# Performance work log

Measured on AMD Instinct MI355X. Metric: run time of the kernel, lower is better.

Reference implementation:

```python
import jax, jax.numpy as jnp
import numpy as np

N_EMBD = 2048
HEAD_DIM = 128
N_CTX = 2048
BATCH = 8
SEQ = 2048


def setup_inputs() -> dict:
    key = jax.random.key(0)
    ks = jax.random.split(key, 7)
    s = 1.0 / np.sqrt(N_EMBD)
    x = jax.random.normal(ks[0], (BATCH, SEQ, N_EMBD), dtype=jnp.float32)
    # torch Linear params: weight (out, in), bias (out,)
    Wq = jax.random.uniform(ks[1], (HEAD_DIM, N_EMBD), jnp.float32, -s, s)
    bq = jax.random.uniform(ks[2], (HEAD_DIM,), jnp.float32, -s, s)
    Wk = jax.random.uniform(ks[3], (HEAD_DIM, N_EMBD), jnp.float32, -s, s)
    bk = jax.random.uniform(ks[4], (HEAD_DIM,), jnp.float32, -s, s)
    Wv = jax.random.uniform(ks[5], (HEAD_DIM, N_EMBD), jnp.float32, -s, s)
    bv = jax.random.uniform(ks[6], (HEAD_DIM,), jnp.float32, -s, s)
    return {"x": x, "Wq": Wq, "bq": bq, "Wk": Wk, "bk": bk, "Wv": Wv, "bv": bv}


def reference(x, Wq, bq, Wk, bk, Wv, bv):
    # projections: y = x @ W^T + b
    q = jnp.einsum('bse,de->bsd', x, Wq) + bq  # (B, S, D)
    k = jnp.einsum('bse,de->bsd', x, Wk) + bk
    v = jnp.einsum('bse,de->bsd', x, Wv) + bv
    seq = x.shape[1]
    scores = jnp.einsum('bqd,bkd->bqk', q, k)  # (B, S, S)
    # causal mask: strictly-upper-triangular positions set to -inf (before scaling, as in source)
    causal = jnp.triu(jnp.ones((seq, seq), dtype=bool), k=1)
    scores = jnp.where(causal[None, :, :], -jnp.inf, scores)
    # NOTE: source scales by sqrt(seq_size), not sqrt(head_dim)
    weight = jax.nn.softmax(scores / jnp.sqrt(jnp.float32(seq)), axis=-1)
    return jnp.einsum('bqk,bkd->bqd', weight, v)
```

## Files before the change

### kernel.cpp

```cpp
#include <hip/hip_runtime.h>
#include <cmath>

#define BATCH 8
#define SEQ   2048
#define NEMB  2048
#define HD    128
#define NROWS (BATCH * SEQ)

typedef __bf16 v8bf __attribute__((ext_vector_type(8)));
typedef float  f32x4 __attribute__((ext_vector_type(4)));

union U8 { v8bf v; __bf16 b[8]; unsigned short e[8]; };
union F4 { f32x4 v; float f[4]; };

__device__ inline void async16(void* lds, const void* g) {
  __builtin_amdgcn_global_load_lds(
      (const __attribute__((address_space(1))) unsigned int*)g,
      (__attribute__((address_space(3))) unsigned int*)lds, 16, 0, 0);
}

__device__ inline v8bf cvt8(float4 a, float4 b) {
  U8 u;
  u.b[0] = (__bf16)a.x; u.b[1] = (__bf16)a.y; u.b[2] = (__bf16)a.z; u.b[3] = (__bf16)a.w;
  u.b[4] = (__bf16)b.x; u.b[5] = (__bf16)b.y; u.b[6] = (__bf16)b.z; u.b[7] = (__bf16)b.w;
  return u.v;
}

__global__ __launch_bounds__(256) void wconv_kernel(
    const float* __restrict__ Wq, const float* __restrict__ Wk,
    const float* __restrict__ Wv, __bf16* __restrict__ out) {
  const int id = blockIdx.x;
  const int proj = id >> 6, blk = id & 63;
  const float* __restrict__ W = proj == 0 ? Wq : proj == 1 ? Wk : Wv;
  __bf16* __restrict__ o = out + (size_t)proj * (HD * NEMB);
  const int base = blk * 4096 + threadIdx.x * 16;
  const float4* s = (const float4*)(W + base);
  float4 f0 = s[0], f1 = s[1], f2 = s[2], f3 = s[3];
  *(v8bf*)(o + base) = cvt8(f0, f1);
  *(v8bf*)(o + base + 8) = cvt8(f2, f3);
}

__global__ __launch_bounds__(256, 3) void qkv_proj_kernel(
    const float* __restrict__ x, const __bf16* __restrict__ Wb,
    const float* __restrict__ bq, const float* __restrict__ bk,
    const float* __restrict__ bv,
    __bf16* __restrict__ Qb, __bf16* __restrict__ Kb, __bf16* __restrict__ Vb)
{
  const int bid0 = blockIdx.x;
  const int bid = ((bid0 & 7) * 96) + (bid0 >> 3);
  const int mt = bid / 3;
  const int proj = bid % 3;
  const __bf16* __restrict__ W = Wb + (size_t)proj * (HD * NEMB);
  const float* __restrict__ bias = proj == 0 ? bq : proj == 1 ? bk : bv;
  __bf16* __restrict__ Out = proj == 0 ? Qb : proj == 1 ? Kb : Vb;
  const int m0 = mt * 64;

  __shared__ float  Asm[64 * 64];
  __shared__ __bf16 Bsm[128 * 64];

  const int t = threadIdx.x, lane = t & 63, w = t >> 6;
  const int wm = w >> 1, wn = w & 1;
  const int hi = lane >> 4, lo = lane & 15;

  const float* pa[4];
  const __bf16* pb[4];
  char* la[4];
  char* lb[4];
#pragma unroll
  for (int i = 0; i < 4; ++i) {
    {
      const int r = (w * 4 + i) * 4 + (lane >> 4);
      const int c = (lane & 15) ^ (r & 7);
      pa[i] = x + (size_t)(m0 + r) * NEMB + c * 4;
      la[i] = (char*)Asm + (w * 4 + i) * 1024;
    }
    {
      const int r = (w * 4 + i) * 8 + (lane >> 3);
      const int c = (lane & 7) ^ (r & 7);
      pb[i] = W + (size_t)r * NEMB + c * 8;
      lb[i] = (char*)Bsm + (w * 4 + i) * 1024;
    }
  }

  f32x4 acc[2][4];
  const f32x4 fz = {0.f, 0.f, 0.f, 0.f};
#pragma unroll
  for (int m = 0; m < 2; ++m)
#pragma unroll
    for (int n = 0; n < 4; ++n) acc[m][n] = fz;

  for (int tt = 0; tt < NEMB / 64; ++tt) {
    const int k0 = tt * 64;
    __syncthreads();
#pragma unroll
    for (int i = 0; i < 4; ++i) async16(la[i], pa[i] + k0);
#pragma unroll
    for (int i = 0; i < 4; ++i) async16(lb[i], pb[i] + k0);
    __syncthreads();

#pragma unroll
    for (int kk = 0; kk < 2; ++kk) {
      v8bf a[2], b[4];
#pragma unroll
      for (int m = 0; m < 2; ++m) {
        const int r = wm * 32 + m * 16 + lo;
        const int s = kk * 8 + hi * 2;
        const char* rowp = (const char*)Asm + r * 256;
        F4 a0, a1;
        a0.v = *(const f32x4*)(rowp + (((s)     ^ (r & 7)) << 4));
        a1.v = *(const f32x4*)(rowp + (((s + 1) ^ (r & 7)) << 4));
        U8 u;
#pragma unroll
        for (int q = 0; q < 4; ++q) {
          u.b[q]     = (__bf16)a0.f[q];
          u.b[q + 4] = (__bf16)a1.f[q];
        }
        a[m] = u.v;
      }
#pragma unroll
      for (int n = 0; n < 4; ++n) {
        const int r = wn * 64 + n * 16 + lo;
        const int kc = kk * 4 + hi;
        b[n] = *(const v8bf*)((const char*)Bsm + r * 128 + ((kc ^ (r & 7)) << 4));
      }
#pragma unroll
      for (int m = 0; m < 2; ++m)
#pragma unroll
        for (int n = 0; n < 4; ++n)
          acc[m][n] = __builtin_amdgcn_mfma_f32_16x16x32_bf16(a[m], b[n], acc[m][n], 0, 0, 0);
    }
  }

#pragma unroll
  for (int n = 0; n < 4; ++n) {
    const int col = wn * 64 + n * 16 + lo;
    const float bi = bias[col];
#pragma unroll
    for (int m = 0; m < 2; ++m) {
#pragma unroll
      for (int r = 0; r < 4; ++r) {
        const int row = m0 + wm * 32 + m * 16 + hi * 4 + r;
        Out[(size_t)row * HD + col] = (__bf16)(acc[m][n][r] + bi);
      }
    }
  }
}

__global__ __launch_bounds__(256) void attn_kernel(
    const __bf16* __restrict__ Qb, const __bf16* __restrict__ Kb,
    const __bf16* __restrict__ Vb, float* __restrict__ Opart,
    float* __restrict__ Ml)
{
  const int bid0 = blockIdx.x;
  const int bid = ((bid0 & 7) << 6) + (bid0 >> 3);
  const int b = bid >> 6;
  const int qs = bid & 63;
  const int qt = qs >> 1;
  const int s  = qs & 1;
  const int q0 = qt * 64;
  const int half = (qt + 2) >> 1;
  const int kv_beg = s ? half : 0;
  const int kv_end = s ? (qt + 1) : half;
  const int nst = kv_end - kv_beg;

  const int t = threadIdx.x, lane = t & 63, w = t >> 6;
  const int hi = lane >> 4, lo = lane & 15;

  __shared__ __bf16 Ksm[2][64 * 128];
  __shared__ __bf16 Vtsm[2][128 * 64];
  __shared__ __bf16 Psm[4][16 * 64];

  v8bf aQ[4];
  {
    const __bf16* qp = Qb + ((size_t)(b * SEQ + q0 + w * 16 + lo)) * HD + hi * 8;
#pragma unroll
    for (int kk = 0; kk < 4; ++kk) aQ[kk] = *(const v8bf*)(qp + kk * 32);
  }

  const __bf16* kga[4];
#pragma unroll
  for (int i = 0; i < 4; ++i) {
    const int r = (w * 4 + i) * 4 + (lane >> 4);
    const int c = (lane & 15) ^ (r & 7);
    kga[i] = Kb + ((size_t)(b * SEQ) + r) * HD + c * 8;
  }

  const int keyg = t >> 4, dg = t & 15;
  U8 vv[4];

  f32x4 accO[8];
  const f32x4 fz = {0.f, 0.f, 0.f, 0.f};
#pragma unroll
  for (int n = 0; n < 8; ++n) accO[n] = fz;
  float m_s[4], l_s[4];
#pragma unroll
  for (int r = 0; r < 4; ++r) { m_s[r] = -INFINITY; l_s[r] = 0.f; }

  const float scale = 0.022097086912079608f;

  if (nst > 0) {
    auto STAGE_K = [&](int kv, int buf) {
      const size_t off = (size_t)kv * 64 * HD;
      char* kb = (char*)&Ksm[buf][0];
#pragma unroll
      for (int i = 0; i < 4; ++i) async16(kb + (w * 4 + i) * 1024, kga[i] + off);
    };
    auto LOAD_V = [&](int kv) {
      const __bf16* vp = Vb + ((size_t)(b * SEQ + kv * 64 + keyg * 4)) * HD + dg * 8;
#pragma unroll
      for (int j = 0; j < 4; ++j) vv[j].v = *(const v8bf*)(vp + (size_t)j * HD);
    };
    auto WRITE_VT = [&](int buf) {
      char* vb2 = (char*)&Vtsm[buf][0];
#pragma unroll
      for (int dd = 0; dd < 8; ++dd) {
        const int d = (dd + dg) & 7;
        ushort4 pk = make_ushort4(vv[0].e[d], vv[1].e[d], vv[2].e[d], vv[3].e[d]);
        const int row = dg * 8 + d;
        *(ushort4*)(vb2 + row * 128 + ((keyg * 8) ^ ((row & 7) << 4))) = pk;
      }
    };

    STAGE_K(kv_beg, 0);
    LOAD_V(kv_beg);
    WRITE_VT(0);
    __syncthreads();

    for (int t2 = 0; t2 < nst; ++t2) {
      const int kv = kv_beg + t2;
      const int cur = t2 & 1;
      const bool more = (t2 + 1 < nst);
      if (more) { STAGE_K(kv + 1, cur ^ 1); LOAD_V(kv + 1); }

      f32x4 accS[4];
#pragma unroll
      for (int n = 0; n < 4; ++n) accS[n] = fz;
      const char* ksm = (const char*)&Ksm[cur][0];
#pragma unroll
      for (int kk = 0; kk < 4; ++kk) {
        const int cb = kk * 64 + hi * 16;
        v8bf bk[4];
#pragma unroll
        for (int n = 0; n < 4; ++n) {
          const int r = n * 16 + lo;
          bk[n] = *(const v8bf*)(ksm + r * 256 + (cb ^ ((r & 7) << 4)));
        }
#pragma unroll
        for (int n = 0; n < 4; ++n)
          accS[n] = __builtin_amdgcn_mfma_f32_16x16x32_bf16(aQ[kk], bk[n], accS[n], 0, 0, 0);
      }

      float sv[4][4];
      const bool diag = (kv == qt);
#pragma unroll
      for (int n = 0; n < 4; ++n)
#pragma unroll
        for (int r = 0; r < 4; ++r) {
          float v = accS[n][r] * scale;
          if (diag) {
            const int key = kv * 64 + n * 16 + lo;
            const int qr = q0 + w * 16 + hi * 4 + r;
            if (key > qr) v = -INFINITY;
          }
          sv[n][r] = v;
        }

      float mx[4];
#pragma unroll
      for (int r = 0; r < 4; ++r) {
        mx[r] = fmaxf(fmaxf(sv[0][r], sv[1][r]), fmaxf(sv[2][r], sv[3][r]));
#pragma unroll
        for (int off = 1; off < 16; off <<= 1)
          mx[r] = fmaxf(mx[r], __shfl_xor(mx[r], off));
      }
      float corr[4], p[4][4], rs[4];
#pragma unroll
      for (int r = 0; r < 4; ++r) {
        const float mnew = fmaxf(m_s[r], mx[r]);
        corr[r] = __expf(m_s[r] - mnew);
        m_s[r] = mnew;
        rs[r] = 0.f;
      }
#pragma unroll
      for (int n = 0; n < 4; ++n)
#pragma unroll
        for (int r = 0; r < 4; ++r) {
          p[n][r] = __expf(sv[n][r] - m_s[r]);
          rs[r] += p[n][r];
        }
#pragma unroll
      for (int r = 0; r < 4; ++r) {
#pragma unroll
        for (int off = 1; off < 16; off <<= 1) rs[r] += __shfl_xor(rs[r], off);
        l_s[r] = l_s[r] * corr[r] + rs[r];
      }
#pragma unroll
      for (int n = 0; n < 8; ++n)
#pragma unroll
        for (int r = 0; r < 4; ++r) accO[n][r] *= corr[r];

#pragma unroll
      for (int n = 0; n < 4; ++n)
#pragma unroll
        for (int r = 0; r < 4; ++r) {
          const int row = hi * 4 + r;
          __bf16 h = (__bf16)p[n][r];
          *(unsigned short*)((char*)&Psm[w][0] + row * 128 +
                             (((n * 16 + lo) * 2) ^ ((row & 7) << 4))) =
              __builtin_bit_cast(unsigned short, h);
        }

      if (more) WRITE_VT(cur ^ 1);

      const char* vsm = (const char*)&Vtsm[cur][0];
#pragma unroll
      for (int k2 = 0; k2 < 2; ++k2) {
        const int cb = k2 * 64 + hi * 16;
        const v8bf aP = *(const v8bf*)((const char*)&Psm[w][0] + lo * 128 + (cb ^ ((lo & 7) << 4)));
#pragma unroll
        for (int n = 0; n < 8; ++n) {
          const int r = n * 16 + lo;
          const v8bf bv = *(const v8bf*)(vsm + r * 128 + (cb ^ ((r & 7) << 4)));
          accO[n] = __builtin_amdgcn_mfma_f32_16x16x32_bf16(aP, bv, accO[n], 0, 0, 0);
        }
      }
      if (more) __syncthreads();
    }
  }

#pragma unroll
  for (int r = 0; r < 4; ++r) {
    const int qr = q0 + w * 16 + hi * 4 + r;
    float* op = Opart + ((size_t)s * NROWS + b * SEQ + qr) * HD + lo;
#pragma unroll
    for (int n = 0; n < 8; ++n) op[n * 16] = accO[n][r];
    if (lo == 0) {
      float* mlp = Ml + ((size_t)s * NROWS + b * SEQ + qr) * 2;
      mlp[0] = m_s[r];
      mlp[1] = l_s[r];
    }
  }
}

__global__ __launch_bounds__(256) void combine_kernel(
    const float* __restrict__ Opart, const float* __restrict__ Ml,
    float* __restrict__ out)
{
  const int idx = blockIdx.x * 256 + threadIdx.x;
  const int row = idx >> 1, h = idx & 1;
  const float m0 = Ml[(size_t)row * 2],           l0 = Ml[(size_t)row * 2 + 1];
  const float m1 = Ml[((size_t)NROWS + row) * 2], l1 = Ml[((size_t)NROWS + row) * 2 + 1];
  const float M = fmaxf(m0, m1);
  const float e0 = __expf(m0 - M), e1 = __expf(m1 - M);
  const float inv = 1.f / (l0 * e0 + l1 * e1);
  const float4* p0 = (const float4*)(Opart + (size_t)row * HD + h * 64);
  const float4* p1 = (const float4*)(Opart + ((size_t)NROWS + row) * HD + h * 64);
  float4* po = (float4*)(out + (size_t)row * HD + h * 64);
#pragma unroll
  for (int j = 0; j < 16; ++j) {
    float4 a = p0[j], c = p1[j];
    float4 r;
    r.x = (a.x * e0 + c.x * e1) * inv;
    r.y = (a.y * e0 + c.y * e1) * inv;
    r.z = (a.z * e0 + c.z * e1) * inv;
    r.w = (a.w * e0 + c.w * e1) * inv;
    po[j] = r;
  }
}

extern "C" void kernel_launch(void* const* d_in, const int* in_sizes, int n_in,
                              void* d_out, int out_size, void* d_ws, size_t ws_size,
                              hipStream_t stream) {
  const float* x  = (const float*)d_in[0];
  const float* Wq = (const float*)d_in[1];
  const float* bq = (const float*)d_in[2];
  const float* Wk = (const float*)d_in[3];
  const float* bk = (const float*)d_in[4];
  const float* Wv = (const float*)d_in[5];
  const float* bv = (const float*)d_in[6];
  float* out = (float*)d_out;

  __bf16* Qb = (__bf16*)d_ws;
  __bf16* Kb = Qb + (size_t)NROWS * HD;
  __bf16* Vb = Kb + (size_t)NROWS * HD;
  __bf16* Wb = Vb + (size_t)NROWS * HD;
  float*  Opart = (float*)(Wb + (size_t)3 * HD * NEMB);
  float*  Ml    = Opart + (size_t)2 * NROWS * HD;

  wconv_kernel<<<dim3(3 * 64), dim3(256), 0, stream>>>(Wq, Wk, Wv, Wb);
  qkv_proj_kernel<<<dim3(256 * 3), dim3(256), 0, stream>>>(
      x, Wb, bq, bk, bv, Qb, Kb, Vb);
  attn_kernel<<<dim3(BATCH * 32 * 2), dim3(256), 0, stream>>>(Qb, Kb, Vb, Opart, Ml);
  combine_kernel<<<dim3(NROWS * 2 / 256), dim3(256), 0, stream>>>(Opart, Ml, out);
}
```

Before: 124.9 us.

## Prepack weights into MFMA fragment layout and load B directly to registers

The weight conversion kernel now writes bf16 weights in the per-lane MFMA fragment order, so the projection kernel can read B operands straight from global memory into registers with coalesced 16-byte loads. This removes the B staging in shared memory. B fragments are double-buffered in registers across k-tiles so the next tile's loads overlap the current MFMAs. The cost is more registers under a 3-blocks-per-SM launch bound and more frequent barriers, since the loop now syncs four times per pair of tiles. Weight loads also bypass LDS reuse and rely on cache hits across blocks.

```diff
diff --git a/kernel.cpp b/kernel.cpp
--- a/kernel.cpp
+++ b/kernel.cpp
@@ -26,22 +26,27 @@
   return u.v;
 }
 
-__global__ __launch_bounds__(256) void wconv_kernel(
+__global__ __launch_bounds__(256) void wpack_kernel(
     const float* __restrict__ Wq, const float* __restrict__ Wk,
     const float* __restrict__ Wv, __bf16* __restrict__ out) {
-  const int id = blockIdx.x;
-  const int proj = id >> 6, blk = id & 63;
-  const float* __restrict__ W = proj == 0 ? Wq : proj == 1 ? Wk : Wv;
-  __bf16* __restrict__ o = out + (size_t)proj * (HD * NEMB);
-  const int base = blk * 4096 + threadIdx.x * 16;
-  const float4* s = (const float4*)(W + base);
-  float4 f0 = s[0], f1 = s[1], f2 = s[2], f3 = s[3];
-  *(v8bf*)(o + base) = cvt8(f0, f1);
-  *(v8bf*)(o + base + 8) = cvt8(f2, f3);
+  const int idx = blockIdx.x * 256 + threadIdx.x;
+  const int lane = idx & 63;
+  const int g = idx >> 6;
+  const int fg = g & 7;
+  const int tt = (g >> 3) & 31;
+  const int wn = (g >> 8) & 1;
+  const int p  = g >> 9;
+  const int n = fg >> 1, kk = fg & 1;
+  const int row = wn * 64 + n * 16 + (lane & 15);
+  const int k   = tt * 64 + kk * 32 + (lane >> 4) * 8;
+  const float* __restrict__ W = p == 0 ? Wq : p == 1 ? Wk : Wv;
+  const float4* s = (const float4*)(W + (size_t)row * NEMB + k);
+  float4 f0 = s[0], f1 = s[1];
+  *(v8bf*)(out + (size_t)idx * 8) = cvt8(f0, f1);
 }
 
 __global__ __launch_bounds__(256, 3) void qkv_proj_kernel(
-    const float* __restrict__ x, const __bf16* __restrict__ Wb,
+    const float* __restrict__ x, const __bf16* __restrict__ Wpack,
     const float* __restrict__ bq, const float* __restrict__ bk,
     const float* __restrict__ bv,
     __bf16* __restrict__ Qb, __bf16* __restrict__ Kb, __bf16* __restrict__ Vb)
@@ -50,37 +55,27 @@
   const int bid = ((bid0 & 7) * 96) + (bid0 >> 3);
   const int mt = bid / 3;
   const int proj = bid % 3;
-  const __bf16* __restrict__ W = Wb + (size_t)proj * (HD * NEMB);
   const float* __restrict__ bias = proj == 0 ? bq : proj == 1 ? bk : bv;
   __bf16* __restrict__ Out = proj == 0 ? Qb : proj == 1 ? Kb : Vb;
   const int m0 = mt * 64;
 
-  __shared__ float  Asm[64 * 64];
-  __shared__ __bf16 Bsm[128 * 64];
+  __shared__ float Asm[64 * 64];
 
   const int t = threadIdx.x, lane = t & 63, w = t >> 6;
   const int wm = w >> 1, wn = w & 1;
   const int hi = lane >> 4, lo = lane & 15;
 
   const float* pa[4];
-  const __bf16* pb[4];
   char* la[4];
-  char* lb[4];
 #pragma unroll
   for (int i = 0; i < 4; ++i) {
-    {
-      const int r = (w * 4 + i) * 4 + (lane >> 4);
-      const int c = (lane & 15) ^ (r & 7);
-      pa[i] = x + (size_t)(m0 + r) * NEMB + c * 4;
-      la[i] = (char*)Asm + (w * 4 + i) * 1024;
-    }
-    {
-      const int r = (w * 4 + i) * 8 + (lane >> 3);
-      const int c = (lane & 7) ^ (r & 7);
-      pb[i] = W + (size_t)r * NEMB + c * 8;
-      lb[i] = (char*)Bsm + (w * 4 + i) * 1024;
-    }
-  }
+    const int r = (w * 4 + i) * 4 + (lane >> 4);
+    const int c = (lane & 15) ^ (r & 7);
+    pa[i] = x + (size_t)(m0 + r) * NEMB + c * 4;
+    la[i] = (char*)Asm + (w * 4 + i) * 1024;
+  }
+
+  const __bf16* bp = Wpack + (size_t)(proj * 2 + wn) * 131072 + lane * 8;
 
   f32x4 acc[2][4];
   const f32x4 fz = {0.f, 0.f, 0.f, 0.f};
@@ -89,18 +84,24 @@
 #pragma unroll
     for (int n = 0; n < 4; ++n) acc[m][n] = fz;
 
-  for (int tt = 0; tt < NEMB / 64; ++tt) {
+  v8bf B0[4][2], B1[4][2];
+  auto LOADB = [&](v8bf (&B)[4][2], int tt) {
+    const __bf16* p = bp + tt * 4096;
+#pragma unroll
+    for (int n = 0; n < 4; ++n)
+#pragma unroll
+      for (int kk = 0; kk < 2; ++kk)
+        B[n][kk] = *(const v8bf*)(p + (n * 2 + kk) * 512);
+  };
+  auto STAGE_A = [&](int tt) {
     const int k0 = tt * 64;
-    __syncthreads();
 #pragma unroll
     for (int i = 0; i < 4; ++i) async16(la[i], pa[i] + k0);
-#pragma unroll
-    for (int i = 0; i < 4; ++i) async16(lb[i], pb[i] + k0);
-    __syncthreads();
-
+  };
+  auto STEP = [&](v8bf (&B)[4][2]) {
 #pragma unroll
     for (int kk = 0; kk < 2; ++kk) {
-      v8bf a[2], b[4];
+      v8bf a[2];
 #pragma unroll
       for (int m = 0; m < 2; ++m) {
         const int r = wm * 32 + m * 16 + lo;
@@ -118,17 +119,26 @@
         a[m] = u.v;
       }
 #pragma unroll
-      for (int n = 0; n < 4; ++n) {
-        const int r = wn * 64 + n * 16 + lo;
-        const int kc = kk * 4 + hi;
-        b[n] = *(const v8bf*)((const char*)Bsm + r * 128 + ((kc ^ (r & 7)) << 4));
-      }
-#pragma unroll
       for (int m = 0; m < 2; ++m)
 #pragma unroll
         for (int n = 0; n < 4; ++n)
-          acc[m][n] = __builtin_amdgcn_mfma_f32_16x16x32_bf16(a[m], b[n], acc[m][n], 0, 0, 0);
+          acc[m][n] = __builtin_amdgcn_mfma_f32_16x16x32_bf16(a[m], B[n][kk], acc[m][n], 0, 0, 0);
     }
+  };
+
+  const int NT = NEMB / 64;
+  LOADB(B0, 0);
+  for (int tt = 0; tt < NT; tt += 2) {
+    __syncthreads();
+    STAGE_A(tt);
+    LOADB(B1, tt + 1);
+    __syncthreads();
+    STEP(B0);
+    __syncthreads();
+    STAGE_A(tt + 1);
+    if (tt + 2 < NT) LOADB(B0, tt + 2);
+    __syncthreads();
+    STEP(B1);
   }
 
 #pragma unroll
@@ -383,13 +393,13 @@
   __bf16* Qb = (__bf16*)d_ws;
   __bf16* Kb = Qb + (size_t)NROWS * HD;
   __bf16* Vb = Kb + (size_t)NROWS * HD;
-  __bf16* Wb = Vb + (size_t)NROWS * HD;
-  float*  Opart = (float*)(Wb + (size_t)3 * HD * NEMB);
+  __bf16* Wpack = Vb + (size_t)NROWS * HD;
+  float*  Opart = (float*)(Wpack + (size_t)3 * HD * NEMB);
   float*  Ml    = Opart + (size_t)2 * NROWS * HD;
 
-  wconv_kernel<<<dim3(3 * 64), dim3(256), 0, stream>>>(Wq, Wk, Wv, Wb);
+  wpack_kernel<<<dim3(384), dim3(256), 0, stream>>>(Wq, Wk, Wv, Wpack);
   qkv_proj_kernel<<<dim3(256 * 3), dim3(256), 0, stream>>>(
-      x, Wb, bq, bk, bv, Qb, Kb, Vb);
+      x, Wpack, bq, bk, bv, Qb, Kb, Vb);
   attn_kernel<<<dim3(BATCH * 32 * 2), dim3(256), 0, stream>>>(Qb, Kb, Vb, Opart, Ml);
   combine_kernel<<<dim3(NROWS * 2 / 256), dim3(256), 0, stream>>>(Opart, Ml, out);
 }
```

Result: slower. 131.4 us (+5.2%).

## Split-K the QKV projection across two warp groups with LDS reduction

Applied to the files above, without the earlier changes.

The QKV projection block grows to 512 threads. Two groups of four warps each handle half of the K dimension, so each group runs 16 iterations instead of 32, using separate LDS buffers (64KB total). After the loop, group 1 writes its partial accumulators to LDS, and group 0 adds them together with the bias before storing. The goal is to shorten the serial K loop and raise the number of waves in flight per block. The costs are a large LDS footprint, which may limit how many blocks fit on a CU, and an extra reduction step through LDS.

```diff
diff --git a/kernel.cpp b/kernel.cpp
--- a/kernel.cpp
+++ b/kernel.cpp
@@ -40,7 +40,7 @@
   *(v8bf*)(o + base + 8) = cvt8(f2, f3);
 }
 
-__global__ __launch_bounds__(256, 3) void qkv_proj_kernel(
+__global__ __launch_bounds__(512, 4) void qkv_proj_kernel(
     const float* __restrict__ x, const __bf16* __restrict__ Wb,
     const float* __restrict__ bq, const float* __restrict__ bk,
     const float* __restrict__ bv,
@@ -55,12 +55,16 @@
   __bf16* __restrict__ Out = proj == 0 ? Qb : proj == 1 ? Kb : Vb;
   const int m0 = mt * 64;
 
-  __shared__ float  Asm[64 * 64];
-  __shared__ __bf16 Bsm[128 * 64];
+  __shared__ char smem[65536];
 
   const int t = threadIdx.x, lane = t & 63, w = t >> 6;
-  const int wm = w >> 1, wn = w & 1;
+  const int kh = w >> 2, wsub = w & 3;
+  const int wm = wsub >> 1, wn = wsub & 1;
   const int hi = lane >> 4, lo = lane & 15;
+  const int kbase = kh * 1024;
+
+  char* Abase = smem + kh * 16384;
+  char* Bbase = smem + 32768 + kh * 16384;
 
   const float* pa[4];
   const __bf16* pb[4];
@@ -69,16 +73,18 @@
 #pragma unroll
   for (int i = 0; i < 4; ++i) {
     {
-      const int r = (w * 4 + i) * 4 + (lane >> 4);
+      const int j = wsub * 4 + i;
+      const int r = j * 4 + (lane >> 4);
       const int c = (lane & 15) ^ (r & 7);
-      pa[i] = x + (size_t)(m0 + r) * NEMB + c * 4;
-      la[i] = (char*)Asm + (w * 4 + i) * 1024;
+      pa[i] = x + (size_t)(m0 + r) * NEMB + kbase + c * 4;
+      la[i] = Abase + j * 1024;
     }
     {
-      const int r = (w * 4 + i) * 8 + (lane >> 3);
+      const int j = wsub * 4 + i;
+      const int r = j * 8 + (lane >> 3);
       const int c = (lane & 7) ^ (r & 7);
-      pb[i] = W + (size_t)r * NEMB + c * 8;
-      lb[i] = (char*)Bsm + (w * 4 + i) * 1024;
+      pb[i] = W + (size_t)r * NEMB + kbase + c * 8;
+      lb[i] = Bbase + j * 1024;
     }
   }
 
@@ -89,7 +95,7 @@
 #pragma unroll
     for (int n = 0; n < 4; ++n) acc[m][n] = fz;
 
-  for (int tt = 0; tt < NEMB / 64; ++tt) {
+  for (int tt = 0; tt < 16; ++tt) {
     const int k0 = tt * 64;
     __syncthreads();
 #pragma unroll
@@ -105,7 +111,7 @@
       for (int m = 0; m < 2; ++m) {
         const int r = wm * 32 + m * 16 + lo;
         const int s = kk * 8 + hi * 2;
-        const char* rowp = (const char*)Asm + r * 256;
+        const char* rowp = (const char*)Abase + r * 256;
         F4 a0, a1;
         a0.v = *(const f32x4*)(rowp + (((s)     ^ (r & 7)) << 4));
         a1.v = *(const f32x4*)(rowp + (((s + 1) ^ (r & 7)) << 4));
@@ -121,7 +127,7 @@
       for (int n = 0; n < 4; ++n) {
         const int r = wn * 64 + n * 16 + lo;
         const int kc = kk * 4 + hi;
-        b[n] = *(const v8bf*)((const char*)Bsm + r * 128 + ((kc ^ (r & 7)) << 4));
+        b[n] = *(const v8bf*)((const char*)Bbase + r * 128 + ((kc ^ (r & 7)) << 4));
       }
 #pragma unroll
       for (int m = 0; m < 2; ++m)
@@ -131,16 +137,33 @@
     }
   }
 
-#pragma unroll
-  for (int n = 0; n < 4; ++n) {
-    const int col = wn * 64 + n * 16 + lo;
-    const float bi = bias[col];
-#pragma unroll
-    for (int m = 0; m < 2; ++m) {
-#pragma unroll
-      for (int r = 0; r < 4; ++r) {
-        const int row = m0 + wm * 32 + m * 16 + hi * 4 + r;
-        Out[(size_t)row * HD + col] = (__bf16)(acc[m][n][r] + bi);
+  __syncthreads();
+  float* red = (float*)smem;
+  if (kh == 1) {
+    float* dst = red + (wsub * 64 + lane) * 32;
+#pragma unroll
+    for (int m = 0; m < 2; ++m)
+#pragma unroll
+      for (int n = 0; n < 4; ++n)
+#pragma unroll
+        for (int r = 0; r < 4; ++r)
+          dst[(m * 4 + n) * 4 + r] = acc[m][n][r];
+  }
+  __syncthreads();
+  if (kh == 0) {
+    const float* src = red + (wsub * 64 + lane) * 32;
+#pragma unroll
+    for (int n = 0; n < 4; ++n) {
+      const int col = wn * 64 + n * 16 + lo;
+      const float bi = bias[col];
+#pragma unroll
+      for (int m = 0; m < 2; ++m) {
+#pragma unroll
+        for (int r = 0; r < 4; ++r) {
+          const int row = m0 + wm * 32 + m * 16 + hi * 4 + r;
+          Out[(size_t)row * HD + col] =
+              (__bf16)(acc[m][n][r] + src[(m * 4 + n) * 4 + r] + bi);
+        }
       }
     }
   }
@@ -388,7 +411,7 @@
   float*  Ml    = Opart + (size_t)2 * NROWS * HD;
 
   wconv_kernel<<<dim3(3 * 64), dim3(256), 0, stream>>>(Wq, Wk, Wv, Wb);
-  qkv_proj_kernel<<<dim3(256 * 3), dim3(256), 0, stream>>>(
+  qkv_proj_kernel<<<dim3(256 * 3), dim3(512), 0, stream>>>(
       x, Wb, bq, bk, bv, Qb, Kb, Vb);
   attn_kernel<<<dim3(BATCH * 32 * 2), dim3(256), 0, stream>>>(Qb, Kb, Vb, Opart, Ml);
   combine_kernel<<<dim3(NROWS * 2 / 256), dim3(256), 0, stream>>>(Opart, Ml, out);
```

Result: slower. 135.8 us (+8.7%).
